# Kernel tuning notes

Measured on AMD Instinct MI355X. Metric: run time of the kernel, lower is better.

## Reference

```python
import jax, jax.numpy as jnp
import numpy as np

NUM_NODES = 32768  # B*N = 16*2048
NUM_REL = 10
NUM_BASES = 4
D = 256
E = 524288


def _rgcn_layer(x, src, dst, rel, basis, comp, root, bias):
    """Basis-decomposed relational GCN layer with per-relation mean aggregation.
    x: [N, Din], basis: [NB, Din, Dout], comp: [R, NB], root: [Din, Dout], bias: [Dout].
    """
    n = x.shape[0]
    # project all nodes through each basis once: [N, NB, Dout]
    xb = jnp.einsum('ni,bio->nbo', x, basis)
    coeff = comp[rel]  # [E, NB] per-edge basis coefficients
    # mean normalization per (destination node, relation) pair
    seg = rel * n + dst  # combined segment id, [E]
    cnt = jax.ops.segment_sum(jnp.ones(rel.shape[0], x.dtype), seg,
                              num_segments=NUM_REL * n)
    inv = jnp.where(cnt > 0, 1.0 / cnt, 0.0)[seg]  # [E]
    # per-edge message: sum_b coeff[e,b] * xb[src_e, b, :] (loop over small NB)
    msg = jnp.zeros((rel.shape[0], basis.shape[2]), x.dtype)
    for b in range(basis.shape[0]):
        msg = msg + coeff[:, b:b + 1] * xb[src, b]
    msg = msg * inv[:, None]
    agg = jax.ops.segment_sum(msg, dst, num_segments=n)  # [N, Dout]
    return agg + x @ root + bias


def setup_inputs() -> dict:
    key = jax.random.key(0)
    ks = jax.random.split(key, 16)
    p = lambda k, shp: (jax.random.normal(k, shp, jnp.float32) * 0.05)
    inp = {
        'x': jax.random.normal(ks[0], (16, 2048, D), jnp.float32),
        't': jax.random.randint(ks[1], (16,), 0, 1000),
        'obj_cond': jax.random.randint(ks[2], (16, 2048), 0, 160),
        'edge_cond': jax.random.randint(ks[3], (2, E), 0, NUM_NODES),
        'relation_cond': jax.random.randint(ks[4], (E,), 0, NUM_REL),
        # layer 0: 256 -> 256 (hidden)
        'basis0': p(ks[5], (NUM_BASES, D, D)),
        'comp0': p(ks[6], (NUM_REL, NUM_BASES)),
        'root0': p(ks[7], (D, D)),
        'bias0': p(ks[8], (D,)),
        # layer 1: 256 -> 256 (output)
        'basis1': p(ks[9], (NUM_BASES, D, D)),
        'comp1': p(ks[10], (NUM_REL, NUM_BASES)),
        'root1': p(ks[11], (D, D)),
        'bias1': p(ks[12], (D,)),
    }
    return inp


def reference(x, t, obj_cond, edge_cond, relation_cond,
              basis0, comp0, root0, bias0, basis1, comp1, root1, bias1):
    B, N, Dm = x.shape
    h = x.reshape(B * N, Dm)
    src, dst = edge_cond[0], edge_cond[1]
    h = _rgcn_layer(h, src, dst, relation_cond, basis0, comp0, root0, bias0)
    h = jax.nn.relu(h)  # hidden-layer activation (dropout disabled at eval)
    h = _rgcn_layer(h, src, dst, relation_cond, basis1, comp1, root1, bias1)
    return h.reshape(B, N, Dm)
```

## Files before the change

### kernel.cpp

```cpp
#include <hip/hip_runtime.h>
#include <stdint.h>

#define NNODES 32768
#define NREL 10
#define NBASES 4
#define DIM 256
#define NEDGE 524288
#define KW 1280
#define KBASE 1024

typedef __attribute__((ext_vector_type(8))) short bf16x8;
typedef __attribute__((ext_vector_type(4))) float f32x4;

__device__ __forceinline__ float bf2f(unsigned short u){
  union { unsigned int i; float f; } v; v.i = ((unsigned int)u) << 16; return v.f;
}
__device__ __forceinline__ unsigned short f2bf(float f){
  union { float f; unsigned int i; } v; v.f = f;
  unsigned int x = v.i;
  unsigned int r = (x + 0x7FFFu + ((x >> 16) & 1u)) >> 16;
  return (unsigned short)r;
}
__device__ __forceinline__ void gll16(const void* g, void* l){
  __builtin_amdgcn_global_load_lds((const __attribute__((address_space(1))) void*)g,
                                   (__attribute__((address_space(3))) void*)l, 16, 0, 0);
}

__global__ __launch_bounds__(256) void conv_kernel(const float* __restrict__ in,
                                                   unsigned short* __restrict__ out)
{
  int i = blockIdx.x * 256 + threadIdx.x;
  float4 v = ((const float4*)in)[i];
  ushort4 o; o.x = f2bf(v.x); o.y = f2bf(v.y); o.z = f2bf(v.z); o.w = f2bf(v.w);
  ((ushort4*)out)[i] = o;
}

__global__ void hist_kernel(const int* __restrict__ ec, const int* __restrict__ rel,
                            int* __restrict__ cnt_rd)
{
  int e = blockIdx.x * 256 + threadIdx.x;
  int d = ec[NEDGE + e];
  int r = rel[e];
  atomicAdd(&cnt_rd[(r << 15) + d], 1);
}

__global__ __launch_bounds__(1024) void scan1(const int* __restrict__ cnt_rd,
                                              int* __restrict__ offs, int* __restrict__ blksum)
{
  __shared__ int sh[1024];
  int tid = threadIdx.x; int gid = blockIdx.x * 1024 + tid;
  int v = 0;
#pragma unroll
  for (int r = 0; r < NREL; r++) v += cnt_rd[(r << 15) + gid];
  sh[tid] = v; __syncthreads();
  for (int off = 1; off < 1024; off <<= 1){
    int t = (tid >= off) ? sh[tid - off] : 0;
    __syncthreads(); sh[tid] += t; __syncthreads();
  }
  offs[gid] = sh[tid] - v;
  if (tid == 1023) blksum[blockIdx.x] = sh[1023];
}
__global__ __launch_bounds__(64) void scan2(int* __restrict__ blksum)
{
  __shared__ int sh[64];
  int tid = threadIdx.x;
  int v = (tid < NNODES / 1024) ? blksum[tid] : 0;
  sh[tid] = v; __syncthreads();
  for (int off = 1; off < 64; off <<= 1){
    int t = (tid >= off) ? sh[tid - off] : 0;
    __syncthreads(); sh[tid] += t; __syncthreads();
  }
  if (tid < NNODES / 1024) blksum[tid] = sh[tid] - v;
}
__global__ __launch_bounds__(1024) void scan3(int* __restrict__ offs, const int* __restrict__ blksum)
{
  int gid = blockIdx.x * 1024 + threadIdx.x;
  offs[gid] += blksum[blockIdx.x];
  if (gid == 0) offs[NNODES] = NEDGE;
}

__global__ void scatter_kernel(const int* __restrict__ ec, const int* __restrict__ rel,
                               const int* __restrict__ offs, int* __restrict__ cursor,
                               unsigned int* __restrict__ meta)
{
  int e = blockIdx.x * 256 + threadIdx.x;
  int s = ec[e];
  int d = ec[NEDGE + e];
  int r = rel[e];
  int p = offs[d] + atomicAdd(&cursor[d], 1);
  meta[p] = ((unsigned int)s << 4) | (unsigned int)r;
}

__global__ __launch_bounds__(256) void build_wt3(
    const float* __restrict__ basis,
    const float* __restrict__ root,
    unsigned short* __restrict__ Wt)
{
  __shared__ float tile[64][65];
  int t = threadIdx.x;
  int k0 = blockIdx.x * 64;
  int n0 = blockIdx.y * 64;
  int tn = t & 63, tk = t >> 6;
#pragma unroll
  for (int i = 0; i < 64; i += 4){
    int k = k0 + tk + i;
    float v = (k < KBASE) ? basis[(size_t)k * 256 + n0 + tn]
                          : root[(size_t)(k - KBASE) * 256 + n0 + tn];
    tile[tk + i][tn] = v;
  }
  __syncthreads();
#pragma unroll
  for (int i = 0; i < 64; i += 4){
    int n = n0 + tk + i;
    Wt[(size_t)n * KW + k0 + tn] = f2bf(tile[tn][tk + i]);
  }
}

__global__ __launch_bounds__(256) void agg5(
    const unsigned short* __restrict__ Xin,
    const int* __restrict__ offs,
    const unsigned int* __restrict__ meta,
    const float* __restrict__ comp,
    const int* __restrict__ cnt_rd,
    unsigned short* __restrict__ z)
{
  __shared__ __attribute__((aligned(16))) float wtab[4][40];
  int t = threadIdx.x;
  int wv = t >> 6, lane = t & 63;
  int d = blockIdx.x * 4 + wv;
  if (lane < 40){
    int r = lane >> 2, b = lane & 3;
    int cnt = cnt_rd[(r << 15) + d];
    wtab[wv][lane] = (cnt > 0) ? comp[r * NBASES + b] / (float)cnt : 0.0f;
  }
  __syncthreads();

  int col = lane * 4;
  const float4* wt4 = (const float4*)&wtab[wv][0];

  float acc[NBASES][4] = {};
  int e0 = offs[d], e1 = offs[d + 1];
  int e = e0;
  for (; e + 3 < e1; e += 4){
    unsigned int m0 = meta[e], m1 = meta[e + 1], m2 = meta[e + 2], m3 = meta[e + 3];
    float4 w0 = wt4[m0 & 15u], w1 = wt4[m1 & 15u], w2 = wt4[m2 & 15u], w3 = wt4[m3 & 15u];
    ushort4 v0 = *(const ushort4*)(Xin + ((size_t)(m0 >> 4)) * 256 + col);
    ushort4 v1 = *(const ushort4*)(Xin + ((size_t)(m1 >> 4)) * 256 + col);
    ushort4 v2 = *(const ushort4*)(Xin + ((size_t)(m2 >> 4)) * 256 + col);
    ushort4 v3 = *(const ushort4*)(Xin + ((size_t)(m3 >> 4)) * 256 + col);
#pragma unroll
    for (int b = 0; b < NBASES; b++){
      float a0 = ((const float*)&w0)[b];
      float a1 = ((const float*)&w1)[b];
      float a2 = ((const float*)&w2)[b];
      float a3 = ((const float*)&w3)[b];
      acc[b][0] += a0 * bf2f(v0.x) + a1 * bf2f(v1.x) + a2 * bf2f(v2.x) + a3 * bf2f(v3.x);
      acc[b][1] += a0 * bf2f(v0.y) + a1 * bf2f(v1.y) + a2 * bf2f(v2.y) + a3 * bf2f(v3.y);
      acc[b][2] += a0 * bf2f(v0.z) + a1 * bf2f(v1.z) + a2 * bf2f(v2.z) + a3 * bf2f(v3.z);
      acc[b][3] += a0 * bf2f(v0.w) + a1 * bf2f(v1.w) + a2 * bf2f(v2.w) + a3 * bf2f(v3.w);
    }
  }
  for (; e < e1; ++e){
    unsigned int md = meta[e];
    float4 w = wt4[md & 15u];
    ushort4 v = *(const ushort4*)(Xin + ((size_t)(md >> 4)) * 256 + col);
#pragma unroll
    for (int b = 0; b < NBASES; b++){
      float a = ((const float*)&w)[b];
      acc[b][0] += a * bf2f(v.x); acc[b][1] += a * bf2f(v.y);
      acc[b][2] += a * bf2f(v.z); acc[b][3] += a * bf2f(v.w);
    }
  }
#pragma unroll
  for (int b = 0; b < NBASES; b++){
    ushort4 o;
    o.x = f2bf(acc[b][0]); o.y = f2bf(acc[b][1]);
    o.z = f2bf(acc[b][2]); o.w = f2bf(acc[b][3]);
    *(ushort4*)(z + (size_t)d * KBASE + b * 256 + col) = o;
  }
}

__global__ __launch_bounds__(256) void gemm5(
    const unsigned short* __restrict__ A0,
    const unsigned short* __restrict__ A1,
    const unsigned short* __restrict__ Wt,
    const float* __restrict__ bias,
    unsigned short* __restrict__ outh,
    float* __restrict__ outf,
    int mode)
{
  __shared__ __attribute__((aligned(16))) short As[128 * 32];
  __shared__ __attribute__((aligned(16))) short Bs[256 * 32];
  int tid  = threadIdx.x;
  int m0   = blockIdx.x * 128;
  int lane = tid & 63;
  int wn   = tid >> 6;
  int lq = lane >> 4, lr = lane & 15;

  f32x4 zero = {0.f, 0.f, 0.f, 0.f};
  f32x4 acc[8][4];
#pragma unroll
  for (int i = 0; i < 8; i++)
#pragma unroll
    for (int j = 0; j < 4; j++) acc[i][j] = zero;

  for (int k0 = 0; k0 < KW; k0 += 32){
    __syncthreads();
#pragma unroll
    for (int i = 0; i < 2; i++){
      int g   = tid + i * 256;
      int row = g >> 2;
      int kc  = ((g & 3) - (g >> 3)) & 3;
      const unsigned short* ga;
      if (k0 < KBASE) ga = A0 + (size_t)(m0 + row) * KBASE + k0 + kc * 8;
      else            ga = A1 + (size_t)(m0 + row) * 256 + (k0 - KBASE) + kc * 8;
      gll16(ga, As + g * 8);
    }
#pragma unroll
    for (int i = 0; i < 4; i++){
      int g   = tid + i * 256;
      int row = g >> 2;
      int kc  = ((g & 3) - (g >> 3)) & 3;
      gll16(Wt + (size_t)row * KW + k0 + kc * 8, Bs + g * 8);
    }
    __syncthreads();

    bf16x8 af[8], bfr[4];
#pragma unroll
    for (int i = 0; i < 8; i++){
      int row = i * 16 + lr;
      af[i] = *(const bf16x8*)(As + row * 32 + (((lq + (row >> 1)) & 3) * 8));
    }
#pragma unroll
    for (int j = 0; j < 4; j++){
      int row = wn * 64 + j * 16 + lr;
      bfr[j] = *(const bf16x8*)(Bs + row * 32 + (((lq + (row >> 1)) & 3) * 8));
    }
#pragma unroll
    for (int i = 0; i < 8; i++)
#pragma unroll
      for (int j = 0; j < 4; j++)
        acc[i][j] = __builtin_amdgcn_mfma_f32_16x16x32_bf16(af[i], bfr[j], acc[i][j], 0, 0, 0);
  }

#pragma unroll
  for (int i = 0; i < 8; i++)
#pragma unroll
    for (int j = 0; j < 4; j++)
#pragma unroll
      for (int r = 0; r < 4; r++){
        int gm = m0 + i * 16 + lq * 4 + r;
        int gn = wn * 64 + j * 16 + lr;
        float v = acc[i][j][r] + bias[gn];
        size_t idx = (size_t)gm * 256 + gn;
        if (mode == 1) outh[idx] = f2bf(fmaxf(v, 0.f));
        else           outf[idx] = v;
      }
}

extern "C" void kernel_launch(void* const* d_in, const int* in_sizes, int n_in,
                              void* d_out, int out_size, void* d_ws, size_t ws_size,
                              hipStream_t stream)
{
  const float* x      = (const float*)d_in[0];
  const int*   ec     = (const int*)d_in[3];
  const int*   rel    = (const int*)d_in[4];
  const float* basis0 = (const float*)d_in[5];
  const float* comp0  = (const float*)d_in[6];
  const float* root0  = (const float*)d_in[7];
  const float* bias0  = (const float*)d_in[8];
  const float* basis1 = (const float*)d_in[9];
  const float* comp1  = (const float*)d_in[10];
  const float* root1  = (const float*)d_in[11];
  const float* bias1  = (const float*)d_in[12];

  char* p = (char*)d_ws;
  unsigned short* z  = (unsigned short*)p; p += (size_t)NNODES * KBASE * 2;
  unsigned short* Xh = (unsigned short*)p; p += (size_t)NNODES * DIM * 2;
  unsigned short* h  = (unsigned short*)p; p += (size_t)NNODES * DIM * 2;
  unsigned short* Wt = (unsigned short*)p; p += (size_t)256 * KW * 2;
  unsigned int* meta = (unsigned int*)p; p += (size_t)NEDGE * 4;
  int* cnt_rd  = (int*)p;   p += (size_t)NREL * NNODES * 4;
  int* cursor  = (int*)p;   p += (size_t)NNODES * 4;
  int* offs    = (int*)p;   p += (size_t)(NNODES + 1) * 4;
  int* blksum  = (int*)p;   p += 1024;

  hipMemsetAsync(cnt_rd, 0, ((size_t)NREL * NNODES + (size_t)NNODES) * 4, stream);

  hist_kernel   <<<NEDGE / 256, 256, 0, stream>>>(ec, rel, cnt_rd);
  scan1         <<<NNODES / 1024, 1024, 0, stream>>>(cnt_rd, offs, blksum);
  scan2         <<<1, 64, 0, stream>>>(blksum);
  scan3         <<<NNODES / 1024, 1024, 0, stream>>>(offs, blksum);
  scatter_kernel<<<NEDGE / 256, 256, 0, stream>>>(ec, rel, offs, cursor, meta);

  conv_kernel<<<(NNODES * DIM / 4) / 256, 256, 0, stream>>>(x, Xh);

  dim3 wgrid(KW / 64, 256 / 64);

  build_wt3<<<wgrid, 256, 0, stream>>>(basis0, root0, Wt);
  agg5<<<NNODES / 4, 256, 0, stream>>>(Xh, offs, meta, comp0, cnt_rd, z);
  gemm5<<<NNODES / 128, 256, 0, stream>>>(z, Xh, Wt, bias0, h, nullptr, 1);

  build_wt3<<<wgrid, 256, 0, stream>>>(basis1, root1, Wt);
  agg5<<<NNODES / 4, 256, 0, stream>>>(h, offs, meta, comp1, cnt_rd, z);
  gemm5<<<NNODES / 128, 256, 0, stream>>>(z, h, Wt, bias1, nullptr, (float*)d_out, 2);
}
```

Baseline: 381.6 us.

## Fuse prep kernels into one launch and halve GEMM row tile

Merges the histogram, fp32-to-bf16 conversion and both layers' weight-transpose builds into a single block-dispatched prep kernel, which removes several launches and lets independent prep work run concurrently. Both layers' packed weights now live in separate buffers so they can be built up front. The GEMM row tile drops from 128 to 64, doubling the grid to 512 blocks for better CU occupancy on the 256-CU part. The cost is less B-tile reuse per block, so the weight matrix is re-read from cache twice as often.

```diff
diff --git a/kernel.cpp b/kernel.cpp
--- a/kernel.cpp
+++ b/kernel.cpp
@@ -9,6 +9,10 @@
 #define KW 1280
 #define KBASE 1024
 
+#define HB 2048
+#define CB 8192
+#define WB 80
+
 typedef __attribute__((ext_vector_type(8))) short bf16x8;
 typedef __attribute__((ext_vector_type(4))) float f32x4;
 
@@ -26,22 +30,51 @@
                                    (__attribute__((address_space(3))) void*)l, 16, 0, 0);
 }
 
-__global__ __launch_bounds__(256) void conv_kernel(const float* __restrict__ in,
-                                                   unsigned short* __restrict__ out)
-{
-  int i = blockIdx.x * 256 + threadIdx.x;
-  float4 v = ((const float4*)in)[i];
-  ushort4 o; o.x = f2bf(v.x); o.y = f2bf(v.y); o.z = f2bf(v.z); o.w = f2bf(v.w);
-  ((ushort4*)out)[i] = o;
-}
-
-__global__ void hist_kernel(const int* __restrict__ ec, const int* __restrict__ rel,
-                            int* __restrict__ cnt_rd)
-{
-  int e = blockIdx.x * 256 + threadIdx.x;
-  int d = ec[NEDGE + e];
-  int r = rel[e];
-  atomicAdd(&cnt_rd[(r << 15) + d], 1);
+__global__ __launch_bounds__(256) void mega_prep(
+    const int* __restrict__ ec, const int* __restrict__ rel,
+    int* __restrict__ cnt_rd,
+    const float* __restrict__ x, unsigned short* __restrict__ Xh,
+    const float* __restrict__ basis0, const float* __restrict__ root0,
+    unsigned short* __restrict__ Wt0,
+    const float* __restrict__ basis1, const float* __restrict__ root1,
+    unsigned short* __restrict__ Wt1)
+{
+  __shared__ float tile[64][65];
+  int bid = blockIdx.x;
+  int t = threadIdx.x;
+  if (bid < HB){
+    int e = bid * 256 + t;
+    int d = ec[NEDGE + e];
+    int r = rel[e];
+    atomicAdd(&cnt_rd[(r << 15) + d], 1);
+  } else if (bid < HB + CB){
+    int i = (bid - HB) * 256 + t;
+    float4 v = ((const float4*)x)[i];
+    ushort4 o; o.x = f2bf(v.x); o.y = f2bf(v.y); o.z = f2bf(v.z); o.w = f2bf(v.w);
+    ((ushort4*)Xh)[i] = o;
+  } else {
+    int b = bid - HB - CB;
+    int layer = b / WB; b %= WB;
+    const float* basis = layer ? basis1 : basis0;
+    const float* root  = layer ? root1  : root0;
+    unsigned short* Wt = layer ? Wt1    : Wt0;
+    int k0 = (b % 20) * 64;
+    int n0 = (b / 20) * 64;
+    int tn = t & 63, tk = t >> 6;
+#pragma unroll
+    for (int i = 0; i < 64; i += 4){
+      int k = k0 + tk + i;
+      float v = (k < KBASE) ? basis[(size_t)k * 256 + n0 + tn]
+                            : root[(size_t)(k - KBASE) * 256 + n0 + tn];
+      tile[tk + i][tn] = v;
+    }
+    __syncthreads();
+#pragma unroll
+    for (int i = 0; i < 64; i += 4){
+      int n = n0 + tk + i;
+      Wt[(size_t)n * KW + k0 + tn] = f2bf(tile[tn][tk + i]);
+    }
+  }
 }
 
 __global__ __launch_bounds__(1024) void scan1(const int* __restrict__ cnt_rd,
@@ -89,31 +122,6 @@
   int r = rel[e];
   int p = offs[d] + atomicAdd(&cursor[d], 1);
   meta[p] = ((unsigned int)s << 4) | (unsigned int)r;
-}
-
-__global__ __launch_bounds__(256) void build_wt3(
-    const float* __restrict__ basis,
-    const float* __restrict__ root,
-    unsigned short* __restrict__ Wt)
-{
-  __shared__ float tile[64][65];
-  int t = threadIdx.x;
-  int k0 = blockIdx.x * 64;
-  int n0 = blockIdx.y * 64;
-  int tn = t & 63, tk = t >> 6;
-#pragma unroll
-  for (int i = 0; i < 64; i += 4){
-    int k = k0 + tk + i;
-    float v = (k < KBASE) ? basis[(size_t)k * 256 + n0 + tn]
-                          : root[(size_t)(k - KBASE) * 256 + n0 + tn];
-    tile[tk + i][tn] = v;
-  }
-  __syncthreads();
-#pragma unroll
-  for (int i = 0; i < 64; i += 4){
-    int n = n0 + tk + i;
-    Wt[(size_t)n * KW + k0 + tn] = f2bf(tile[tn][tk + i]);
-  }
 }
 
 __global__ __launch_bounds__(256) void agg5(
@@ -180,7 +188,7 @@
   }
 }
 
-__global__ __launch_bounds__(256) void gemm5(
+__global__ __launch_bounds__(256) void gemm4(
     const unsigned short* __restrict__ A0,
     const unsigned short* __restrict__ A1,
     const unsigned short* __restrict__ Wt,
@@ -189,45 +197,44 @@
     float* __restrict__ outf,
     int mode)
 {
-  __shared__ __attribute__((aligned(16))) short As[128 * 32];
+  __shared__ __attribute__((aligned(16))) short As[64 * 32];
   __shared__ __attribute__((aligned(16))) short Bs[256 * 32];
   int tid  = threadIdx.x;
-  int m0   = blockIdx.x * 128;
+  int m0   = blockIdx.x * 64;
   int lane = tid & 63;
   int wn   = tid >> 6;
   int lq = lane >> 4, lr = lane & 15;
 
   f32x4 zero = {0.f, 0.f, 0.f, 0.f};
-  f32x4 acc[8][4];
-#pragma unroll
-  for (int i = 0; i < 8; i++)
+  f32x4 acc[4][4];
+#pragma unroll
+  for (int i = 0; i < 4; i++)
 #pragma unroll
     for (int j = 0; j < 4; j++) acc[i][j] = zero;
+
+  int arow = tid >> 2;
+  int akc  = ((tid & 3) - (tid >> 3)) & 3;
 
   for (int k0 = 0; k0 < KW; k0 += 32){
     __syncthreads();
-#pragma unroll
-    for (int i = 0; i < 2; i++){
-      int g   = tid + i * 256;
-      int row = g >> 2;
-      int kc  = ((g & 3) - (g >> 3)) & 3;
+    {
       const unsigned short* ga;
-      if (k0 < KBASE) ga = A0 + (size_t)(m0 + row) * KBASE + k0 + kc * 8;
-      else            ga = A1 + (size_t)(m0 + row) * 256 + (k0 - KBASE) + kc * 8;
-      gll16(ga, As + g * 8);
+      if (k0 < KBASE) ga = A0 + (size_t)(m0 + arow) * KBASE + k0 + akc * 8;
+      else            ga = A1 + (size_t)(m0 + arow) * 256 + (k0 - KBASE) + akc * 8;
+      gll16(ga, As + tid * 8);
     }
 #pragma unroll
     for (int i = 0; i < 4; i++){
-      int g   = tid + i * 256;
-      int row = g >> 2;
-      int kc  = ((g & 3) - (g >> 3)) & 3;
-      gll16(Wt + (size_t)row * KW + k0 + kc * 8, Bs + g * 8);
+      int gb  = tid + i * 256;
+      int row = gb >> 2;
+      int kc  = ((gb & 3) - (gb >> 3)) & 3;
+      gll16(Wt + (size_t)row * KW + k0 + kc * 8, Bs + gb * 8);
     }
     __syncthreads();
 
-    bf16x8 af[8], bfr[4];
-#pragma unroll
-    for (int i = 0; i < 8; i++){
+    bf16x8 af[4], bfr[4];
+#pragma unroll
+    for (int i = 0; i < 4; i++){
       int row = i * 16 + lr;
       af[i] = *(const bf16x8*)(As + row * 32 + (((lq + (row >> 1)) & 3) * 8));
     }
@@ -237,14 +244,14 @@
       bfr[j] = *(const bf16x8*)(Bs + row * 32 + (((lq + (row >> 1)) & 3) * 8));
     }
 #pragma unroll
-    for (int i = 0; i < 8; i++)
+    for (int i = 0; i < 4; i++)
 #pragma unroll
       for (int j = 0; j < 4; j++)
         acc[i][j] = __builtin_amdgcn_mfma_f32_16x16x32_bf16(af[i], bfr[j], acc[i][j], 0, 0, 0);
   }
 
 #pragma unroll
-  for (int i = 0; i < 8; i++)
+  for (int i = 0; i < 4; i++)
 #pragma unroll
     for (int j = 0; j < 4; j++)
 #pragma unroll
@@ -275,11 +282,12 @@
   const float* bias1  = (const float*)d_in[12];
 
   char* p = (char*)d_ws;
-  unsigned short* z  = (unsigned short*)p; p += (size_t)NNODES * KBASE * 2;
-  unsigned short* Xh = (unsigned short*)p; p += (size_t)NNODES * DIM * 2;
-  unsigned short* h  = (unsigned short*)p; p += (size_t)NNODES * DIM * 2;
-  unsigned short* Wt = (unsigned short*)p; p += (size_t)256 * KW * 2;
-  unsigned int* meta = (unsigned int*)p; p += (size_t)NEDGE * 4;
+  unsigned short* z   = (unsigned short*)p; p += (size_t)NNODES * KBASE * 2;
+  unsigned short* Xh  = (unsigned short*)p; p += (size_t)NNODES * DIM * 2;
+  unsigned short* h   = (unsigned short*)p; p += (size_t)NNODES * DIM * 2;
+  unsigned short* Wt0 = (unsigned short*)p; p += (size_t)256 * KW * 2;
+  unsigned short* Wt1 = (unsigned short*)p; p += (size_t)256 * KW * 2;
+  unsigned int* meta  = (unsigned int*)p;   p += (size_t)NEDGE * 4;
   int* cnt_rd  = (int*)p;   p += (size_t)NREL * NNODES * 4;
   int* cursor  = (int*)p;   p += (size_t)NNODES * 4;
   int* offs    = (int*)p;   p += (size_t)(NNODES + 1) * 4;
@@ -287,21 +295,17 @@
 
   hipMemsetAsync(cnt_rd, 0, ((size_t)NREL * NNODES + (size_t)NNODES) * 4, stream);
 
-  hist_kernel   <<<NEDGE / 256, 256, 0, stream>>>(ec, rel, cnt_rd);
-  scan1         <<<NNODES / 1024, 1024, 0, stream>>>(cnt_rd, offs, blksum);
-  scan2         <<<1, 64, 0, stream>>>(blksum);
-  scan3         <<<NNODES / 1024, 1024, 0, stream>>>(offs, blksum);
+  mega_prep<<<HB + CB + 2 * WB, 256, 0, stream>>>(
+      ec, rel, cnt_rd, x, Xh, basis0, root0, Wt0, basis1, root1, Wt1);
+
+  scan1<<<NNODES / 1024, 1024, 0, stream>>>(cnt_rd, offs, blksum);
+  scan2<<<1, 64, 0, stream>>>(blksum);
+  scan3<<<NNODES / 1024, 1024, 0, stream>>>(offs, blksum);
   scatter_kernel<<<NEDGE / 256, 256, 0, stream>>>(ec, rel, offs, cursor, meta);
 
-  conv_kernel<<<(NNODES * DIM / 4) / 256, 256, 0, stream>>>(x, Xh);
-
-  dim3 wgrid(KW / 64, 256 / 64);
-
-  build_wt3<<<wgrid, 256, 0, stream>>>(basis0, root0, Wt);
   agg5<<<NNODES / 4, 256, 0, stream>>>(Xh, offs, meta, comp0, cnt_rd, z);
-  gemm5<<<NNODES / 128, 256, 0, stream>>>(z, Xh, Wt, bias0, h, nullptr, 1);
-
-  build_wt3<<<wgrid, 256, 0, stream>>>(basis1, root1, Wt);
+  gemm4<<<NNODES / 64, 256, 0, stream>>>(z, Xh, Wt0, bias0, h, nullptr, 1);
+
   agg5<<<NNODES / 4, 256, 0, stream>>>(h, offs, meta, comp1, cnt_rd, z);
-  gemm5<<<NNODES / 128, 256, 0, stream>>>(z, h, Wt, bias1, nullptr, (float*)d_out, 2);
-}
+  gemm4<<<NNODES / 64, 256, 0, stream>>>(z, h, Wt1, bias1, nullptr, (float*)d_out, 2);
+}
```

Result: faster. 330.1 us (-13.5%).
